# Optimization experiments

Hardware: AMD Instinct MI355X
Metric: run time of the kernel (lower is better)

Reference implementation:

```python
import jax, jax.numpy as jnp
import numpy as np

N_NODES = 100000
N_EDGES = 600000
F_IN = 128
F_OUT = 128


def setup_inputs() -> dict:
    key = jax.random.key(0)
    ks = jax.random.split(key, 9)
    stdv = 1.0 / np.sqrt(F_OUT)
    return {
        "x": jax.random.normal(ks[0], (N_NODES, F_IN), dtype=jnp.float32),
        "weight": jax.random.uniform(ks[1], (F_IN, F_OUT), dtype=jnp.float32, minval=-stdv, maxval=stdv),
        "bias": jax.random.uniform(ks[2], (F_OUT,), dtype=jnp.float32, minval=-stdv, maxval=stdv),
        "vals0": jax.random.uniform(ks[3], (N_EDGES,), dtype=jnp.float32),
        "vals1": jax.random.uniform(ks[4], (N_EDGES,), dtype=jnp.float32),
        "rows0": jax.random.randint(ks[5], (N_EDGES,), 0, N_NODES, dtype=jnp.int32),
        "cols0": jax.random.randint(ks[6], (N_EDGES,), 0, N_NODES, dtype=jnp.int32),
        "rows1": jax.random.randint(ks[7], (N_EDGES,), 0, N_NODES, dtype=jnp.int32),
        "cols1": jax.random.randint(ks[8], (N_EDGES,), 0, N_NODES, dtype=jnp.int32),
    }


def _spmm(rows, cols, vals, dense, n):
    # COO sparse [n,n] @ dense [n,f]: gather source rows, scale, scatter-add to dest rows
    msgs = dense[cols] * vals[:, None]          # [E, f]
    return jax.ops.segment_sum(msgs, rows, num_segments=n)


def reference(x, weight, bias, vals0, vals1, rows0, cols0, rows1, cols1):
    n = x.shape[0]
    support = x @ weight                         # [N, F_OUT] dense GEMM
    out = _spmm(rows0, cols0, vals0, support, n) \
        + _spmm(rows1, cols1, vals1, support, n)
    return out + bias
```

## Files before the change

kernel.cpp:

```cpp
#include <hip/hip_runtime.h>


#define FDIM 128
#define EPB 2048

typedef __attribute__((ext_vector_type(8))) short short8;
typedef __attribute__((ext_vector_type(4))) float floatx4;

__device__ __forceinline__ unsigned short f32_to_bf16(float f) {
    unsigned int u = __float_as_uint(f);
    unsigned int r = u + 0x7fffu + ((u >> 16) & 1u);
    return (unsigned short)(r >> 16);
}

__device__ __forceinline__ float bf16_lo(unsigned int u) {
    return __uint_as_float((u & 0xffffu) << 16);
}
__device__ __forceinline__ float bf16_hi(unsigned int u) {
    return __uint_as_float(u & 0xffff0000u);
}

__global__ __launch_bounds__(256) void prep(const float* __restrict__ w,
                                            unsigned short* __restrict__ wt,
                                            int* __restrict__ zero_ptr, int zero_ints) {
    int bid = blockIdx.x;
    if (bid < 64) {
        int idx = bid * 256 + threadIdx.x;
        int nn = idx >> 7, k = idx & 127;
        wt[idx] = f32_to_bf16(w[(size_t)k * FDIM + nn]);
    } else {
        int idx = (bid - 64) * 256 + threadIdx.x;
        if (idx < zero_ints) zero_ptr[idx] = 0;
    }
}

__global__ __launch_bounds__(256) void hist_rows(const int* __restrict__ rows0,
                                                 const int* __restrict__ rows1,
                                                 int* __restrict__ count, int E) {
    int gid = blockIdx.x * 256 + threadIdx.x;
    if (gid >= 2 * E) return;
    int r = (gid < E) ? rows0[gid] : rows1[gid - E];
    atomicAdd(&count[r], 1);
}

__global__ __launch_bounds__(256) void gemm_lds(const float* __restrict__ x,
                                                const unsigned short* __restrict__ wt,
                                                unsigned short* __restrict__ support,
                                                int n) {
    __shared__ __align__(16) short Bs[128][136];
    const int tid = threadIdx.x;

    #pragma unroll
    for (int i = 0; i < 8; ++i) {
        int idx = tid + i * 256;
        int r = idx >> 4, c8 = idx & 15;
        *(short8*)&Bs[r][c8 * 8] = *(const short8*)(wt + (size_t)r * FDIM + c8 * 8);
    }
    __syncthreads();

    const int wv = tid >> 6, lane = tid & 63;
    const int quad = lane >> 4, lr = lane & 15;
    const int row0 = blockIdx.x * 64 + wv * 16;
    if (row0 >= n) return;

    const int arow = row0 + lr;
    const bool rowok = arow < n;
    const float* xr = x + (size_t)arow * FDIM;

    float4 f[8];
    #pragma unroll
    for (int ks = 0; ks < 4; ++ks) {
        f[2 * ks]     = rowok ? *(const float4*)(xr + ks * 32 + quad * 8)     : make_float4(0.f,0.f,0.f,0.f);
        f[2 * ks + 1] = rowok ? *(const float4*)(xr + ks * 32 + quad * 8 + 4) : make_float4(0.f,0.f,0.f,0.f);
    }

    floatx4 acc[8];
    #pragma unroll
    for (int nt = 0; nt < 8; ++nt) acc[nt] = (floatx4)0.f;

    #pragma unroll
    for (int ks = 0; ks < 4; ++ks) {
        float4 lo = f[2 * ks], hi = f[2 * ks + 1];
        short8 a;
        a[0] = (short)f32_to_bf16(lo.x); a[1] = (short)f32_to_bf16(lo.y);
        a[2] = (short)f32_to_bf16(lo.z); a[3] = (short)f32_to_bf16(lo.w);
        a[4] = (short)f32_to_bf16(hi.x); a[5] = (short)f32_to_bf16(hi.y);
        a[6] = (short)f32_to_bf16(hi.z); a[7] = (short)f32_to_bf16(hi.w);
        #pragma unroll
        for (int nt = 0; nt < 8; ++nt) {
            short8 b = *(const short8*)&Bs[nt * 16 + lr][ks * 32 + quad * 8];
            acc[nt] = __builtin_amdgcn_mfma_f32_16x16x32_bf16(a, b, acc[nt], 0, 0, 0);
        }
    }

    #pragma unroll
    for (int i = 0; i < 4; ++i) {
        int row = row0 + quad * 4 + i;
        if (row < n) {
            #pragma unroll
            for (int nt = 0; nt < 8; ++nt)
                support[(size_t)row * FDIM + nt * 16 + lr] = f32_to_bf16(acc[nt][i]);
        }
    }
}

__device__ __forceinline__ int block_incl_scan(int v, int tid, int* lds) {
    int lane = tid & 63, wv = tid >> 6;
    #pragma unroll
    for (int d = 1; d < 64; d <<= 1) {
        int y = __shfl_up(v, d);
        if (lane >= d) v += y;
    }
    if (lane == 63) lds[wv] = v;
    __syncthreads();
    if (wv == 0 && lane < 4) {
        int s = lds[lane];
        #pragma unroll
        for (int d = 1; d < 4; d <<= 1) {
            int y = __shfl_up(s, d);
            if (lane >= d) s += y;
        }
        lds[4 + lane] = s;
    }
    __syncthreads();
    int add = (wv > 0) ? lds[4 + wv - 1] : 0;
    return v + add;
}

__global__ __launch_bounds__(256) void rowptr_scan(const int* __restrict__ count,
                                                   int* __restrict__ rowptr,
                                                   int* __restrict__ cursor,
                                                   int* __restrict__ gcur, int n) {
    __shared__ int lds[8];
    __shared__ int base;
    int tid = threadIdx.x;
    int idx = blockIdx.x * 256 + tid;
    int v = (idx < n) ? count[idx] : 0;
    int inc = block_incl_scan(v, tid, lds);
    if (tid == 255) base = atomicAdd(gcur, inc);
    __syncthreads();
    if (idx < n) {
        int p = base + inc - v;
        rowptr[idx] = p;
        cursor[idx] = p;
    }
}

__global__ __launch_bounds__(256) void scatter_cur(
    const int* __restrict__ rows0, const int* __restrict__ cols0, const float* __restrict__ vals0,
    const int* __restrict__ rows1, const int* __restrict__ cols1, const float* __restrict__ vals1,
    int* __restrict__ cursor,
    int2* __restrict__ rec, int E, int nper) {
    const int p = blockIdx.x & 7;
    const int rlo = p * nper;
    const int base = (blockIdx.x >> 3) * EPB;
    const int tid = threadIdx.x;
    #pragma unroll
    for (int it = 0; it < EPB / 256; ++it) {
        int gid = base + it * 256 + tid;
        if (gid < 2 * E) {
            int r = (gid < E) ? rows0[gid] : rows1[gid - E];
            if ((unsigned)(r - rlo) < (unsigned)nper) {
                int c; float v;
                if (gid < E) { c = cols0[gid]; v = vals0[gid]; }
                else         { int e = gid - E; c = cols1[e]; v = vals1[e]; }
                int pos = atomicAdd(&cursor[r], 1);
                rec[pos] = make_int2(c, __float_as_int(v));
            }
        }
    }
}

__global__ __launch_bounds__(256) void pull_csr(const unsigned short* __restrict__ support,
                                                const int* __restrict__ rowptr,
                                                const int* __restrict__ cursor,
                                                const int2* __restrict__ rec,
                                                const float* __restrict__ bias,
                                                float* __restrict__ out, int n) {
    int wid = (blockIdx.x * 256 + threadIdx.x) >> 6;
    int lane = threadIdx.x & 63;
    if (wid >= n) return;
    int beg = rowptr[wid];
    int end = cursor[wid];
    float ax = 0.f, ay = 0.f;
    const char* sp = (const char*)support;
    const unsigned loff = (unsigned)lane << 2;

    for (int base = beg; base < end; base += 64) {
        int m = end - base; if (m > 64) m = 64;
        long long pk = 0;
        if (lane < m) pk = *(const long long*)&rec[base + lane];
        int j = 0;
        for (; j + 8 <= m; j += 8) {
            long long p0 = __shfl(pk, j);
            long long p1 = __shfl(pk, j + 1);
            long long p2 = __shfl(pk, j + 2);
            long long p3 = __shfl(pk, j + 3);
            long long p4 = __shfl(pk, j + 4);
            long long p5 = __shfl(pk, j + 5);
            long long p6 = __shfl(pk, j + 6);
            long long p7 = __shfl(pk, j + 7);
            unsigned u0 = *(const unsigned*)(sp + (((unsigned)p0) << 8) + loff);
            unsigned u1 = *(const unsigned*)(sp + (((unsigned)p1) << 8) + loff);
            unsigned u2 = *(const unsigned*)(sp + (((unsigned)p2) << 8) + loff);
            unsigned u3 = *(const unsigned*)(sp + (((unsigned)p3) << 8) + loff);
            unsigned u4 = *(const unsigned*)(sp + (((unsigned)p4) << 8) + loff);
            unsigned u5 = *(const unsigned*)(sp + (((unsigned)p5) << 8) + loff);
            unsigned u6 = *(const unsigned*)(sp + (((unsigned)p6) << 8) + loff);
            unsigned u7 = *(const unsigned*)(sp + (((unsigned)p7) << 8) + loff);
            float v0 = __int_as_float((int)(p0 >> 32));
            float v1 = __int_as_float((int)(p1 >> 32));
            float v2 = __int_as_float((int)(p2 >> 32));
            float v3 = __int_as_float((int)(p3 >> 32));
            float v4 = __int_as_float((int)(p4 >> 32));
            float v5 = __int_as_float((int)(p5 >> 32));
            float v6 = __int_as_float((int)(p6 >> 32));
            float v7 = __int_as_float((int)(p7 >> 32));
            ax += v0 * bf16_lo(u0); ay += v0 * bf16_hi(u0);
            ax += v1 * bf16_lo(u1); ay += v1 * bf16_hi(u1);
            ax += v2 * bf16_lo(u2); ay += v2 * bf16_hi(u2);
            ax += v3 * bf16_lo(u3); ay += v3 * bf16_hi(u3);
            ax += v4 * bf16_lo(u4); ay += v4 * bf16_hi(u4);
            ax += v5 * bf16_lo(u5); ay += v5 * bf16_hi(u5);
            ax += v6 * bf16_lo(u6); ay += v6 * bf16_hi(u6);
            ax += v7 * bf16_lo(u7); ay += v7 * bf16_hi(u7);
        }
        for (; j + 4 <= m; j += 4) {
            long long p0 = __shfl(pk, j);
            long long p1 = __shfl(pk, j + 1);
            long long p2 = __shfl(pk, j + 2);
            long long p3 = __shfl(pk, j + 3);
            unsigned u0 = *(const unsigned*)(sp + (((unsigned)p0) << 8) + loff);
            unsigned u1 = *(const unsigned*)(sp + (((unsigned)p1) << 8) + loff);
            unsigned u2 = *(const unsigned*)(sp + (((unsigned)p2) << 8) + loff);
            unsigned u3 = *(const unsigned*)(sp + (((unsigned)p3) << 8) + loff);
            float v0 = __int_as_float((int)(p0 >> 32));
            float v1 = __int_as_float((int)(p1 >> 32));
            float v2 = __int_as_float((int)(p2 >> 32));
            float v3 = __int_as_float((int)(p3 >> 32));
            ax += v0 * bf16_lo(u0); ay += v0 * bf16_hi(u0);
            ax += v1 * bf16_lo(u1); ay += v1 * bf16_hi(u1);
            ax += v2 * bf16_lo(u2); ay += v2 * bf16_hi(u2);
            ax += v3 * bf16_lo(u3); ay += v3 * bf16_hi(u3);
        }
        for (; j < m; ++j) {
            long long p = __shfl(pk, j);
            unsigned u = *(const unsigned*)(sp + (((unsigned)p) << 8) + loff);
            float v = __int_as_float((int)(p >> 32));
            ax += v * bf16_lo(u); ay += v * bf16_hi(u);
        }
    }
    float2 b = *(const float2*)(bias + lane * 2);
    *(float2*)(out + (size_t)wid * FDIM + lane * 2) = make_float2(ax + b.x, ay + b.y);
}

__global__ __launch_bounds__(256) void init_bias(const float* __restrict__ bias,
                                                 float* __restrict__ out, int n) {
    int idx = blockIdx.x * 256 + threadIdx.x;
    int total = n * (FDIM / 4);
    if (idx < total) {
        int j = (idx & (FDIM / 4 - 1)) * 4;
        float4 b = *(const float4*)(bias + j);
        *(float4*)(out + (size_t)idx * 4) = b;
    }
}

__global__ __launch_bounds__(256) void scatter_bf16(
    const unsigned short* __restrict__ support,
    const int* __restrict__ rows0, const int* __restrict__ cols0, const float* __restrict__ vals0,
    const int* __restrict__ rows1, const int* __restrict__ cols1, const float* __restrict__ vals1,
    float* __restrict__ out, int E) {
    int gid = blockIdx.x * 256 + threadIdx.x;
    int lane = gid & 63;
    int eg = gid >> 6;
    if (eg >= 2 * E) return;
    int r, c; float v;
    if (eg < E) { r = rows0[eg]; c = cols0[eg]; v = vals0[eg]; }
    else        { int e = eg - E; r = rows1[e]; c = cols1[e]; v = vals1[e]; }
    unsigned int u = *(const unsigned int*)(support + (size_t)c * FDIM + lane * 2);
    float sx = bf16_lo(u);
    float sy = bf16_hi(u);
    float* op = out + (size_t)r * FDIM + lane * 2;
    atomicAdd(op,     sx * v);
    atomicAdd(op + 1, sy * v);
}

static inline size_t align256(size_t v) { return (v + 255) & ~(size_t)255; }

extern "C" void kernel_launch(void* const* d_in, const int* in_sizes, int n_in,
                              void* d_out, int out_size, void* d_ws, size_t ws_size,
                              hipStream_t stream) {
    const float* x     = (const float*)d_in[0];
    const float* w     = (const float*)d_in[1];
    const float* bias  = (const float*)d_in[2];
    const float* vals0 = (const float*)d_in[3];
    const float* vals1 = (const float*)d_in[4];
    const int*   rows0 = (const int*)d_in[5];
    const int*   cols0 = (const int*)d_in[6];
    const int*   rows1 = (const int*)d_in[7];
    const int*   cols1 = (const int*)d_in[8];
    const int n = in_sizes[0] / FDIM;
    const int E = in_sizes[3];
    float* out = (float*)d_out;

    const int NB = (n + 255) / 256;

    size_t off = 0;
    unsigned short* support = (unsigned short*)((char*)d_ws + off);
    off = align256(off + (size_t)n * FDIM * 2);
    unsigned short* wt = (unsigned short*)((char*)d_ws + off);
    off = align256(off + (size_t)FDIM * FDIM * 2);
    size_t count_off = off;
    int*  count  = (int*)((char*)d_ws + off);  off = align256(off + (size_t)n * 4);
    int*  gcur   = (int*)((char*)d_ws + off);  off = align256(off + 4);
    size_t zero_bytes = off - count_off;
    int*  rowptr = (int*)((char*)d_ws + off);  off = align256(off + (size_t)n * 4);
    int*  cursor = (int*)((char*)d_ws + off);  off = align256(off + (size_t)n * 4);
    int2* rec    = (int2*)((char*)d_ws + off); off = align256(off + (size_t)2 * E * 8);

    const bool fits = off <= ws_size;

    int zero_ints = fits ? (int)(zero_bytes / 4) : 0;
    int zb = (zero_ints + 255) / 256;
    prep<<<64 + zb, 256, 0, stream>>>(w, wt, (int*)((char*)d_ws + count_off), zero_ints);

    gemm_lds<<<(n + 63) / 64, 256, 0, stream>>>(x, wt, support, n);

    if (fits) {
        int eb = (2 * E + 255) / 256;
        hist_rows<<<eb, 256, 0, stream>>>(rows0, rows1, count, E);
        rowptr_scan<<<NB, 256, 0, stream>>>(count, rowptr, cursor, gcur, n);
        int nper = (n + 7) / 8;
        int ntiles = (2 * E + EPB - 1) / EPB;
        scatter_cur<<<ntiles * 8, 256, 0, stream>>>(rows0, cols0, vals0,
                                                    rows1, cols1, vals1,
                                                    cursor, rec, E, nper);
        pull_csr<<<(n + 3) / 4, 256, 0, stream>>>(support, rowptr, cursor, rec, bias, out, n);
    } else {
        int total4 = n * (FDIM / 4);
        init_bias<<<(total4 + 255) / 256, 256, 0, stream>>>(bias, out, n);
        long long tthreads = 2LL * E * 64;
        int blocks = (int)((tthreads + 255) / 256);
        scatter_bf16<<<blocks, 256, 0, stream>>>(support, rows0, cols0, vals0,
                                                 rows1, cols1, vals1, out, E);
    }
}
```

Before: 287.1 us.

## Fuse GEMM with CSR scatter and record per-edge ranks in histogram pass

The histogram pass now stores each edge's atomic rank, so the scatter computes positions as rowptr+rank instead of doing a second round of atomics on a cursor array. The GEMM and the scatter are merged into one launch whose blocks are interleaved (three scatter groups per GEMM group), so the compute-bound GEMM and the memory-bound scatter can overlap. The weight transpose joins the histogram launch, and zeroing moves to hipMemsetAsync. The cost is an extra 2E-int rank array to write and read, plus more complex block indexing.

```diff
diff --git a/kernel.cpp b/kernel.cpp
--- a/kernel.cpp
+++ b/kernel.cpp
@@ -20,35 +20,99 @@
     return __uint_as_float(u & 0xffff0000u);
 }
 
-__global__ __launch_bounds__(256) void prep(const float* __restrict__ w,
-                                            unsigned short* __restrict__ wt,
-                                            int* __restrict__ zero_ptr, int zero_ints) {
+__global__ __launch_bounds__(256) void hist_prep(const int* __restrict__ rows0,
+                                                 const int* __restrict__ rows1,
+                                                 int* __restrict__ count,
+                                                 int* __restrict__ rank, int E,
+                                                 const float* __restrict__ w,
+                                                 unsigned short* __restrict__ wt,
+                                                 int HB) {
     int bid = blockIdx.x;
-    if (bid < 64) {
-        int idx = bid * 256 + threadIdx.x;
+    if (bid < HB) {
+        int gid = bid * 256 + threadIdx.x;
+        if (gid < 2 * E) {
+            int r = (gid < E) ? rows0[gid] : rows1[gid - E];
+            rank[gid] = atomicAdd(&count[r], 1);
+        }
+    } else {
+        int idx = (bid - HB) * 256 + threadIdx.x;
         int nn = idx >> 7, k = idx & 127;
         wt[idx] = f32_to_bf16(w[(size_t)k * FDIM + nn]);
-    } else {
-        int idx = (bid - 64) * 256 + threadIdx.x;
-        if (idx < zero_ints) zero_ptr[idx] = 0;
-    }
-}
-
-__global__ __launch_bounds__(256) void hist_rows(const int* __restrict__ rows0,
-                                                 const int* __restrict__ rows1,
-                                                 int* __restrict__ count, int E) {
-    int gid = blockIdx.x * 256 + threadIdx.x;
-    if (gid >= 2 * E) return;
-    int r = (gid < E) ? rows0[gid] : rows1[gid - E];
-    atomicAdd(&count[r], 1);
-}
-
-__global__ __launch_bounds__(256) void gemm_lds(const float* __restrict__ x,
-                                                const unsigned short* __restrict__ wt,
-                                                unsigned short* __restrict__ support,
-                                                int n) {
+    }
+}
+
+__device__ __forceinline__ int block_incl_scan(int v, int tid, int* lds) {
+    int lane = tid & 63, wv = tid >> 6;
+    #pragma unroll
+    for (int d = 1; d < 64; d <<= 1) {
+        int y = __shfl_up(v, d);
+        if (lane >= d) v += y;
+    }
+    if (lane == 63) lds[wv] = v;
+    __syncthreads();
+    if (wv == 0 && lane < 4) {
+        int s = lds[lane];
+        #pragma unroll
+        for (int d = 1; d < 4; d <<= 1) {
+            int y = __shfl_up(s, d);
+            if (lane >= d) s += y;
+        }
+        lds[4 + lane] = s;
+    }
+    __syncthreads();
+    int add = (wv > 0) ? lds[4 + wv - 1] : 0;
+    return v + add;
+}
+
+__global__ __launch_bounds__(256) void rowptr_scan(const int* __restrict__ count,
+                                                   int* __restrict__ rowptr,
+                                                   int* __restrict__ gcur, int n) {
+    __shared__ int lds[8];
+    __shared__ int base;
+    int tid = threadIdx.x;
+    int idx = blockIdx.x * 256 + tid;
+    int v = (idx < n) ? count[idx] : 0;
+    int inc = block_incl_scan(v, tid, lds);
+    if (tid == 255) base = atomicAdd(gcur, inc);
+    __syncthreads();
+    if (idx < n) rowptr[idx] = base + inc - v;
+}
+
+__global__ __launch_bounds__(256) void gemm_scatter(
+    const float* __restrict__ x, const unsigned short* __restrict__ wt,
+    unsigned short* __restrict__ support, int n,
+    const int* __restrict__ rows0, const int* __restrict__ cols0, const float* __restrict__ vals0,
+    const int* __restrict__ rows1, const int* __restrict__ cols1, const float* __restrict__ vals1,
+    const int* __restrict__ rank, const int* __restrict__ rowptr,
+    int2* __restrict__ rec, int E, int nper, int ntiles) {
     __shared__ __align__(16) short Bs[128][136];
     const int tid = threadIdx.x;
+    const int g = blockIdx.x >> 3, w = blockIdx.x & 7;
+
+    if ((g & 3) != 3) {
+        const int sg = (g >> 2) * 3 + (g & 3);
+        if (sg >= ntiles) return;
+        const int rlo = w * nper;
+        const int base = sg * EPB;
+        #pragma unroll
+        for (int it = 0; it < EPB / 256; ++it) {
+            int gid = base + it * 256 + tid;
+            if (gid < 2 * E) {
+                int r = (gid < E) ? rows0[gid] : rows1[gid - E];
+                if ((unsigned)(r - rlo) < (unsigned)nper) {
+                    int c; float v;
+                    if (gid < E) { c = cols0[gid]; v = vals0[gid]; }
+                    else         { int e = gid - E; c = cols1[e]; v = vals1[e]; }
+                    rec[rowptr[r] + rank[gid]] = make_int2(c, __float_as_int(v));
+                }
+            }
+        }
+        return;
+    }
+
+    const int gid64 = (g >> 2) * 8 + w;
+    const int bro = gid64 * 64;
+    if (bro >= n) return;
 
     #pragma unroll
     for (int i = 0; i < 8; ++i) {
@@ -60,7 +124,7 @@
 
     const int wv = tid >> 6, lane = tid & 63;
     const int quad = lane >> 4, lr = lane & 15;
-    const int row0 = blockIdx.x * 64 + wv * 16;
+    const int row0 = bro + wv * 16;
     if (row0 >= n) return;
 
     const int arow = row0 + lr;
@@ -104,76 +168,9 @@
     }
 }
 
-__device__ __forceinline__ int block_incl_scan(int v, int tid, int* lds) {
-    int lane = tid & 63, wv = tid >> 6;
-    #pragma unroll
-    for (int d = 1; d < 64; d <<= 1) {
-        int y = __shfl_up(v, d);
-        if (lane >= d) v += y;
-    }
-    if (lane == 63) lds[wv] = v;
-    __syncthreads();
-    if (wv == 0 && lane < 4) {
-        int s = lds[lane];
-        #pragma unroll
-        for (int d = 1; d < 4; d <<= 1) {
-            int y = __shfl_up(s, d);
-            if (lane >= d) s += y;
-        }
-        lds[4 + lane] = s;
-    }
-    __syncthreads();
-    int add = (wv > 0) ? lds[4 + wv - 1] : 0;
-    return v + add;
-}
-
-__global__ __launch_bounds__(256) void rowptr_scan(const int* __restrict__ count,
-                                                   int* __restrict__ rowptr,
-                                                   int* __restrict__ cursor,
-                                                   int* __restrict__ gcur, int n) {
-    __shared__ int lds[8];
-    __shared__ int base;
-    int tid = threadIdx.x;
-    int idx = blockIdx.x * 256 + tid;
-    int v = (idx < n) ? count[idx] : 0;
-    int inc = block_incl_scan(v, tid, lds);
-    if (tid == 255) base = atomicAdd(gcur, inc);
-    __syncthreads();
-    if (idx < n) {
-        int p = base + inc - v;
-        rowptr[idx] = p;
-        cursor[idx] = p;
-    }
-}
-
-__global__ __launch_bounds__(256) void scatter_cur(
-    const int* __restrict__ rows0, const int* __restrict__ cols0, const float* __restrict__ vals0,
-    const int* __restrict__ rows1, const int* __restrict__ cols1, const float* __restrict__ vals1,
-    int* __restrict__ cursor,
-    int2* __restrict__ rec, int E, int nper) {
-    const int p = blockIdx.x & 7;
-    const int rlo = p * nper;
-    const int base = (blockIdx.x >> 3) * EPB;
-    const int tid = threadIdx.x;
-    #pragma unroll
-    for (int it = 0; it < EPB / 256; ++it) {
-        int gid = base + it * 256 + tid;
-        if (gid < 2 * E) {
-            int r = (gid < E) ? rows0[gid] : rows1[gid - E];
-            if ((unsigned)(r - rlo) < (unsigned)nper) {
-                int c; float v;
-                if (gid < E) { c = cols0[gid]; v = vals0[gid]; }
-                else         { int e = gid - E; c = cols1[e]; v = vals1[e]; }
-                int pos = atomicAdd(&cursor[r], 1);
-                rec[pos] = make_int2(c, __float_as_int(v));
-            }
-        }
-    }
-}
-
 __global__ __launch_bounds__(256) void pull_csr(const unsigned short* __restrict__ support,
                                                 const int* __restrict__ rowptr,
-                                                const int* __restrict__ cursor,
+                                                const int* __restrict__ count,
                                                 const int2* __restrict__ rec,
                                                 const float* __restrict__ bias,
                                                 float* __restrict__ out, int n) {
@@ -181,7 +178,7 @@
     int lane = threadIdx.x & 63;
     if (wid >= n) return;
     int beg = rowptr[wid];
-    int end = cursor[wid];
+    int end = beg + count[wid];
     float ax = 0.f, ay = 0.f;
     const char* sp = (const char*)support;
     const unsigned loff = (unsigned)lane << 2;
@@ -254,6 +251,67 @@
     *(float2*)(out + (size_t)wid * FDIM + lane * 2) = make_float2(ax + b.x, ay + b.y);
 }
 
+__global__ __launch_bounds__(256) void wt_only(const float* __restrict__ w,
+                                               unsigned short* __restrict__ wt) {
+    int idx = blockIdx.x * 256 + threadIdx.x;
+    int nn = idx >> 7, k = idx & 127;
+    wt[idx] = f32_to_bf16(w[(size_t)k * FDIM + nn]);
+}
+
+__global__ __launch_bounds__(256) void gemm_only(const float* __restrict__ x,
+                                                 const unsigned short* __restrict__ wt,
+                                                 unsigned short* __restrict__ support,
+                                                 int n) {
+    __shared__ __align__(16) short Bs[128][136];
+    const int tid = threadIdx.x;
+    #pragma unroll
+    for (int i = 0; i < 8; ++i) {
+        int idx = tid + i * 256;
+        int r = idx >> 4, c8 = idx & 15;
+        *(short8*)&Bs[r][c8 * 8] = *(const short8*)(wt + (size_t)r * FDIM + c8 * 8);
+    }
+    __syncthreads();
+    const int wv = tid >> 6, lane = tid & 63;
+    const int quad = lane >> 4, lr = lane & 15;
+    const int row0 = blockIdx.x * 64 + wv * 16;
+    if (row0 >= n) return;
+    const int arow = row0 + lr;
+    const bool rowok = arow < n;
+    const float* xr = x + (size_t)arow * FDIM;
+    float4 f[8];
+    #pragma unroll
+    for (int ks = 0; ks < 4; ++ks) {
+        f[2 * ks]     = rowok ? *(const float4*)(xr + ks * 32 + quad * 8)     : make_float4(0.f,0.f,0.f,0.f);
+        f[2 * ks + 1] = rowok ? *(const float4*)(xr + ks * 32 + quad * 8 + 4) : make_float4(0.f,0.f,0.f,0.f);
+    }
+    floatx4 acc[8];
+    #pragma unroll
+    for (int nt = 0; nt < 8; ++nt) acc[nt] = (floatx4)0.f;
+    #pragma unroll
+    for (int ks = 0; ks < 4; ++ks) {
+        float4 lo = f[2 * ks], hi = f[2 * ks + 1];
+        short8 a;
+        a[0] = (short)f32_to_bf16(lo.x); a[1] = (short)f32_to_bf16(lo.y);
+        a[2] = (short)f32_to_bf16(lo.z); a[3] = (short)f32_to_bf16(lo.w);
+        a[4] = (short)f32_to_bf16(hi.x); a[5] = (short)f32_to_bf16(hi.y);
+        a[6] = (short)f32_to_bf16(hi.z); a[7] = (short)f32_to_bf16(hi.w);
+        #pragma unroll
+        for (int nt = 0; nt < 8; ++nt) {
+            short8 b = *(const short8*)&Bs[nt * 16 + lr][ks * 32 + quad * 8];
+            acc[nt] = __builtin_amdgcn_mfma_f32_16x16x32_bf16(a, b, acc[nt], 0, 0, 0);
+        }
+    }
+    #pragma unroll
+    for (int i = 0; i < 4; ++i) {
+        int row = row0 + quad * 4 + i;
+        if (row < n) {
+            #pragma unroll
+            for (int nt = 0; nt < 8; ++nt)
+                support[(size_t)row * FDIM + nt * 16 + lr] = f32_to_bf16(acc[nt][i]);
+        }
+    }
+}
+
 __global__ __launch_bounds__(256) void init_bias(const float* __restrict__ bias,
                                                  float* __restrict__ out, int n) {
     int idx = blockIdx.x * 256 + threadIdx.x;
@@ -315,28 +373,31 @@
     int*  gcur   = (int*)((char*)d_ws + off);  off = align256(off + 4);
     size_t zero_bytes = off - count_off;
     int*  rowptr = (int*)((char*)d_ws + off);  off = align256(off + (size_t)n * 4);
-    int*  cursor = (int*)((char*)d_ws + off);  off = align256(off + (size_t)n * 4);
+    int*  rank   = (int*)((char*)d_ws + off);  off = align256(off + (size_t)2 * E * 4);
     int2* rec    = (int2*)((char*)d_ws + off); off = align256(off + (size_t)2 * E * 8);
 
     const bool fits = off <= ws_size;
 
-    int zero_ints = fits ? (int)(zero_bytes / 4) : 0;
-    int zb = (zero_ints + 255) / 256;
-    prep<<<64 + zb, 256, 0, stream>>>(w, wt, (int*)((char*)d_ws + count_off), zero_ints);
-
-    gemm_lds<<<(n + 63) / 64, 256, 0, stream>>>(x, wt, support, n);
-
     if (fits) {
-        int eb = (2 * E + 255) / 256;
-        hist_rows<<<eb, 256, 0, stream>>>(rows0, rows1, count, E);
-        rowptr_scan<<<NB, 256, 0, stream>>>(count, rowptr, cursor, gcur, n);
-        int nper = (n + 7) / 8;
-        int ntiles = (2 * E + EPB - 1) / EPB;
-        scatter_cur<<<ntiles * 8, 256, 0, stream>>>(rows0, cols0, vals0,
-                                                    rows1, cols1, vals1,
-                                                    cursor, rec, E, nper);
-        pull_csr<<<(n + 3) / 4, 256, 0, stream>>>(support, rowptr, cursor, rec, bias, out, n);
+        hipMemsetAsync((char*)d_ws + count_off, 0, zero_bytes, stream);
+        const int HB = (2 * E + 255) / 256;
+        hist_prep<<<HB + 64, 256, 0, stream>>>(rows0, rows1, count, rank, E, w, wt, HB);
+        rowptr_scan<<<NB, 256, 0, stream>>>(count, rowptr, gcur, n);
+
+        const int nper   = (n + 7) / 8;
+        const int ntiles = (2 * E + EPB - 1) / EPB;
+        const int gemmB  = (n + 63) / 64;
+        int c = (ntiles + 2) / 3;
+        int c2 = (gemmB + 7) / 8;
+        if (c2 > c) c = c2;
+        gemm_scatter<<<c * 32, 256, 0, stream>>>(x, wt, support, n,
+                                                 rows0, cols0, vals0,
+                                                 rows1, cols1, vals1,
+                                                 rank, rowptr, rec, E, nper, ntiles);
+        pull_csr<<<(n + 3) / 4, 256, 0, stream>>>(support, rowptr, count, rec, bias, out, n);
     } else {
+        wt_only<<<(FDIM * FDIM) / 256, 256, 0, stream>>>(w, wt);
+        gemm_only<<<(n + 63) / 64, 256, 0, stream>>>(x, wt, support, n);
         int total4 = n * (FDIM / 4);
         init_bias<<<(total4 + 255) / 256, 256, 0, stream>>>(bias, out, n);
         long long tthreads = 2LL * E * 64;
```

New measurement: 287.4 us. No clear change (+0.1%).

## Record per-edge rank in histogram to drop scatter atomics and merge prep kernels

Applied to the files above, without the earlier changes.

The histogram kernel now saves each edge's atomic return value as its rank within its row, so the scatter pass writes to rowptr[r]+rank with no second atomic. The cursor array goes away; pull_csr computes the row end from count. The weight transpose is folded into the histogram launch, and zeroing now uses hipMemsetAsync, which removes a separate kernel launch. The trade-off is an extra 2E-int rank array that must be written and later read back.

```diff
diff --git a/kernel.cpp b/kernel.cpp
--- a/kernel.cpp
+++ b/kernel.cpp
@@ -20,27 +20,62 @@
     return __uint_as_float(u & 0xffff0000u);
 }
 
-__global__ __launch_bounds__(256) void prep(const float* __restrict__ w,
-                                            unsigned short* __restrict__ wt,
-                                            int* __restrict__ zero_ptr, int zero_ints) {
+__global__ __launch_bounds__(256) void hist_prep(const int* __restrict__ rows0,
+                                                 const int* __restrict__ rows1,
+                                                 int* __restrict__ count,
+                                                 int* __restrict__ rank, int E,
+                                                 const float* __restrict__ w,
+                                                 unsigned short* __restrict__ wt,
+                                                 int HB) {
     int bid = blockIdx.x;
-    if (bid < 64) {
-        int idx = bid * 256 + threadIdx.x;
+    if (bid < HB) {
+        int gid = bid * 256 + threadIdx.x;
+        if (gid < 2 * E) {
+            int r = (gid < E) ? rows0[gid] : rows1[gid - E];
+            rank[gid] = atomicAdd(&count[r], 1);
+        }
+    } else {
+        int idx = (bid - HB) * 256 + threadIdx.x;
         int nn = idx >> 7, k = idx & 127;
         wt[idx] = f32_to_bf16(w[(size_t)k * FDIM + nn]);
-    } else {
-        int idx = (bid - 64) * 256 + threadIdx.x;
-        if (idx < zero_ints) zero_ptr[idx] = 0;
-    }
-}
-
-__global__ __launch_bounds__(256) void hist_rows(const int* __restrict__ rows0,
-                                                 const int* __restrict__ rows1,
-                                                 int* __restrict__ count, int E) {
-    int gid = blockIdx.x * 256 + threadIdx.x;
-    if (gid >= 2 * E) return;
-    int r = (gid < E) ? rows0[gid] : rows1[gid - E];
-    atomicAdd(&count[r], 1);
+    }
+}
+
+__device__ __forceinline__ int block_incl_scan(int v, int tid, int* lds) {
+    int lane = tid & 63, wv = tid >> 6;
+    #pragma unroll
+    for (int d = 1; d < 64; d <<= 1) {
+        int y = __shfl_up(v, d);
+        if (lane >= d) v += y;
+    }
+    if (lane == 63) lds[wv] = v;
+    __syncthreads();
+    if (wv == 0 && lane < 4) {
+        int s = lds[lane];
+        #pragma unroll
+        for (int d = 1; d < 4; d <<= 1) {
+            int y = __shfl_up(s, d);
+            if (lane >= d) s += y;
+        }
+        lds[4 + lane] = s;
+    }
+    __syncthreads();
+    int add = (wv > 0) ? lds[4 + wv - 1] : 0;
+    return v + add;
+}
+
+__global__ __launch_bounds__(256) void rowptr_scan(const int* __restrict__ count,
+                                                   int* __restrict__ rowptr,
+                                                   int* __restrict__ gcur, int n) {
+    __shared__ int lds[8];
+    __shared__ int base;
+    int tid = threadIdx.x;
+    int idx = blockIdx.x * 256 + tid;
+    int v = (idx < n) ? count[idx] : 0;
+    int inc = block_incl_scan(v, tid, lds);
+    if (tid == 255) base = atomicAdd(gcur, inc);
+    __syncthreads();
+    if (idx < n) rowptr[idx] = base + inc - v;
 }
 
 __global__ __launch_bounds__(256) void gemm_lds(const float* __restrict__ x,
@@ -104,52 +139,10 @@
     }
 }
 
-__device__ __forceinline__ int block_incl_scan(int v, int tid, int* lds) {
-    int lane = tid & 63, wv = tid >> 6;
-    #pragma unroll
-    for (int d = 1; d < 64; d <<= 1) {
-        int y = __shfl_up(v, d);
-        if (lane >= d) v += y;
-    }
-    if (lane == 63) lds[wv] = v;
-    __syncthreads();
-    if (wv == 0 && lane < 4) {
-        int s = lds[lane];
-        #pragma unroll
-        for (int d = 1; d < 4; d <<= 1) {
-            int y = __shfl_up(s, d);
-            if (lane >= d) s += y;
-        }
-        lds[4 + lane] = s;
-    }
-    __syncthreads();
-    int add = (wv > 0) ? lds[4 + wv - 1] : 0;
-    return v + add;
-}
-
-__global__ __launch_bounds__(256) void rowptr_scan(const int* __restrict__ count,
-                                                   int* __restrict__ rowptr,
-                                                   int* __restrict__ cursor,
-                                                   int* __restrict__ gcur, int n) {
-    __shared__ int lds[8];
-    __shared__ int base;
-    int tid = threadIdx.x;
-    int idx = blockIdx.x * 256 + tid;
-    int v = (idx < n) ? count[idx] : 0;
-    int inc = block_incl_scan(v, tid, lds);
-    if (tid == 255) base = atomicAdd(gcur, inc);
-    __syncthreads();
-    if (idx < n) {
-        int p = base + inc - v;
-        rowptr[idx] = p;
-        cursor[idx] = p;
-    }
-}
-
-__global__ __launch_bounds__(256) void scatter_cur(
+__global__ __launch_bounds__(256) void scatter_row(
     const int* __restrict__ rows0, const int* __restrict__ cols0, const float* __restrict__ vals0,
     const int* __restrict__ rows1, const int* __restrict__ cols1, const float* __restrict__ vals1,
-    int* __restrict__ cursor,
+    const int* __restrict__ rank, const int* __restrict__ rowptr,
     int2* __restrict__ rec, int E, int nper) {
     const int p = blockIdx.x & 7;
     const int rlo = p * nper;
@@ -164,8 +157,7 @@
                 int c; float v;
                 if (gid < E) { c = cols0[gid]; v = vals0[gid]; }
                 else         { int e = gid - E; c = cols1[e]; v = vals1[e]; }
-                int pos = atomicAdd(&cursor[r], 1);
-                rec[pos] = make_int2(c, __float_as_int(v));
+                rec[rowptr[r] + rank[gid]] = make_int2(c, __float_as_int(v));
             }
         }
     }
@@ -173,7 +165,7 @@
 
 __global__ __launch_bounds__(256) void pull_csr(const unsigned short* __restrict__ support,
                                                 const int* __restrict__ rowptr,
-                                                const int* __restrict__ cursor,
+                                                const int* __restrict__ count,
                                                 const int2* __restrict__ rec,
                                                 const float* __restrict__ bias,
                                                 float* __restrict__ out, int n) {
@@ -181,7 +173,7 @@
     int lane = threadIdx.x & 63;
     if (wid >= n) return;
     int beg = rowptr[wid];
-    int end = cursor[wid];
+    int end = beg + count[wid];
     float ax = 0.f, ay = 0.f;
     const char* sp = (const char*)support;
     const unsigned loff = (unsigned)lane << 2;
@@ -254,6 +246,13 @@
     *(float2*)(out + (size_t)wid * FDIM + lane * 2) = make_float2(ax + b.x, ay + b.y);
 }
 
+__global__ __launch_bounds__(256) void wt_only(const float* __restrict__ w,
+                                               unsigned short* __restrict__ wt) {
+    int idx = blockIdx.x * 256 + threadIdx.x;
+    int nn = idx >> 7, k = idx & 127;
+    wt[idx] = f32_to_bf16(w[(size_t)k * FDIM + nn]);
+}
+
 __global__ __launch_bounds__(256) void init_bias(const float* __restrict__ bias,
                                                  float* __restrict__ out, int n) {
     int idx = blockIdx.x * 256 + threadIdx.x;
@@ -315,28 +314,27 @@
     int*  gcur   = (int*)((char*)d_ws + off);  off = align256(off + 4);
     size_t zero_bytes = off - count_off;
     int*  rowptr = (int*)((char*)d_ws + off);  off = align256(off + (size_t)n * 4);
-    int*  cursor = (int*)((char*)d_ws + off);  off = align256(off + (size_t)n * 4);
+    int*  rank   = (int*)((char*)d_ws + off);  off = align256(off + (size_t)2 * E * 4);
     int2* rec    = (int2*)((char*)d_ws + off); off = align256(off + (size_t)2 * E * 8);
 
     const bool fits = off <= ws_size;
 
-    int zero_ints = fits ? (int)(zero_bytes / 4) : 0;
-    int zb = (zero_ints + 255) / 256;
-    prep<<<64 + zb, 256, 0, stream>>>(w, wt, (int*)((char*)d_ws + count_off), zero_ints);
-
-    gemm_lds<<<(n + 63) / 64, 256, 0, stream>>>(x, wt, support, n);
-
     if (fits) {
-        int eb = (2 * E + 255) / 256;
-        hist_rows<<<eb, 256, 0, stream>>>(rows0, rows1, count, E);
-        rowptr_scan<<<NB, 256, 0, stream>>>(count, rowptr, cursor, gcur, n);
-        int nper = (n + 7) / 8;
-        int ntiles = (2 * E + EPB - 1) / EPB;
-        scatter_cur<<<ntiles * 8, 256, 0, stream>>>(rows0, cols0, vals0,
+        hipMemsetAsync((char*)d_ws + count_off, 0, zero_bytes, stream);
+        const int HB = (2 * E + 255) / 256;
+        hist_prep<<<HB + 64, 256, 0, stream>>>(rows0, rows1, count, rank, E, w, wt, HB);
+        rowptr_scan<<<NB, 256, 0, stream>>>(count, rowptr, gcur, n);
+        gemm_lds<<<(n + 63) / 64, 256, 0, stream>>>(x, wt, support, n);
+
+        const int nper   = (n + 7) / 8;
+        const int ntiles = (2 * E + EPB - 1) / EPB;
+        scatter_row<<<ntiles * 8, 256, 0, stream>>>(rows0, cols0, vals0,
                                                     rows1, cols1, vals1,
-                                                    cursor, rec, E, nper);
-        pull_csr<<<(n + 3) / 4, 256, 0, stream>>>(support, rowptr, cursor, rec, bias, out, n);
+                                                    rank, rowptr, rec, E, nper);
+        pull_csr<<<(n + 3) / 4, 256, 0, stream>>>(support, rowptr, count, rec, bias, out, n);
     } else {
+        wt_only<<<(FDIM * FDIM) / 256, 256, 0, stream>>>(w, wt);
+        gemm_lds<<<(n + 63) / 64, 256, 0, stream>>>(x, wt, support, n);
         int total4 = n * (FDIM / 4);
         init_bias<<<(total4 + 255) / 256, 256, 0, stream>>>(bias, out, n);
         long long tthreads = 2LL * E * 64;
```

New measurement: 273.1 us. -4.9%, faster.
